# Kernel optimization log

Measured on AMD Instinct MI355X. Metric: run time of the kernel, lower is better.

Reference implementation:

```python
import jax, jax.numpy as jnp
from jax import lax
import numpy as np

B, L, D = 2, 2048, 768
DI, DS, DTR, K = 1536, 16, 48, 4  # d_inner, d_state, dt_rank, d_conv
EPS = 1e-5


def layernorm(x, g, b):
    mu = jnp.mean(x, axis=-1, keepdims=True)
    var = jnp.mean(jnp.square(x - mu), axis=-1, keepdims=True)
    return (x - mu) * lax.rsqrt(var + EPS) * g + b


def mamba(x, in_w, conv_w, conv_b, xproj_w, dt_w, dt_b, A_log, Dp, out_w):
    # x: [B, L, D]
    xz = x @ in_w.T                       # [B, L, 2*DI]
    xc, z = jnp.split(xz, 2, axis=-1)     # [B, L, DI] each
    # causal depthwise conv1d, kernel K, left pad K-1, truncate to L
    xp = jnp.pad(xc, ((0, 0), (K - 1, 0), (0, 0)))
    conv = conv_b + sum(xp[:, k:k + L, :] * conv_w[:, k] for k in range(K))
    xc = jax.nn.silu(conv)
    dbc = xc @ xproj_w.T                  # [B, L, DTR+2*DS]
    dt = dbc[..., :DTR]
    Bm = dbc[..., DTR:DTR + DS]           # [B, L, DS]
    Cm = dbc[..., DTR + DS:]              # [B, L, DS]
    dt = jax.nn.softplus(dt @ dt_w.T + dt_b)  # [B, L, DI]
    A = -jnp.exp(A_log)                   # [DI, DS]

    def step(h, inp):
        dt_t, B_t, C_t, x_t = inp         # [B,DI], [B,DS], [B,DS], [B,DI]
        dA = jnp.exp(dt_t[..., None] * A)               # [B, DI, DS]
        h = dA * h + (dt_t * x_t)[..., None] * B_t[:, None, :]
        y = jnp.einsum('bds,bs->bd', h, C_t)
        return h, y

    h0 = jnp.zeros((x.shape[0], DI, DS), x.dtype)
    _, ys = lax.scan(step, h0, (dt.transpose(1, 0, 2), Bm.transpose(1, 0, 2),
                                Cm.transpose(1, 0, 2), xc.transpose(1, 0, 2)))
    y = ys.transpose(1, 0, 2) + xc * Dp   # [B, L, DI]
    y = y * jax.nn.silu(z)
    return y @ out_w.T                    # [B, L, D]


def setup_inputs() -> dict:
    key = jax.random.key(0)
    ks = iter(jax.random.split(key, 40))
    r = lambda s, sc=0.02: jax.random.normal(next(ks), s, jnp.float32) * sc
    A0 = jnp.log(jnp.broadcast_to(jnp.arange(1, DS + 1, dtype=jnp.float32), (DI, DS)))
    def mamba_params(p):
        return {
            f'{p}_in_w': r((2 * DI, D)), f'{p}_conv_w': r((DI, K), 0.2),
            f'{p}_conv_b': jnp.zeros((DI,)), f'{p}_xproj_w': r((DTR + 2 * DS, DI)),
            f'{p}_dt_w': r((DI, DTR), 0.1), f'{p}_dt_b': jnp.zeros((DI,)),
            f'{p}_A_log': A0, f'{p}_D': jnp.ones((DI,)), f'{p}_out_w': r((D, DI)),
        }
    inp = {'x': jax.random.normal(next(ks), (B, L, D), jnp.float32),
           'norm_g': jnp.ones((D,)), 'norm_b': jnp.zeros((D,))}
    inp.update(mamba_params('f'))
    inp.update(mamba_params('b'))
    inp.update({'mix_w': r((D, 2 * D)), 'mix_b': jnp.zeros((D,)),
                'ffn_w1': r((4 * D, D)), 'ffn_b1': jnp.zeros((4 * D,)),
                'ffn_w2': r((D, 4 * D)), 'ffn_b2': jnp.zeros((D,)),
                'ffn_norm_g': jnp.ones((D,)), 'ffn_norm_b': jnp.zeros((D,))})
    return inp


def reference(x, norm_g, norm_b,
              f_in_w, f_conv_w, f_conv_b, f_xproj_w, f_dt_w, f_dt_b, f_A_log, f_D, f_out_w,
              b_in_w, b_conv_w, b_conv_b, b_xproj_w, b_dt_w, b_dt_b, b_A_log, b_D, b_out_w,
              mix_w, mix_b, ffn_w1, ffn_b1, ffn_w2, ffn_b2, ffn_norm_g, ffn_norm_b):
    residual = x
    xn = layernorm(x, norm_g, norm_b)
    xf = mamba(xn, f_in_w, f_conv_w, f_conv_b, f_xproj_w, f_dt_w, f_dt_b, f_A_log, f_D, f_out_w)
    xb = mamba(jnp.flip(xn, axis=1), b_in_w, b_conv_w, b_conv_b, b_xproj_w,
               b_dt_w, b_dt_b, b_A_log, b_D, b_out_w)
    xb = jnp.flip(xb, axis=1)
    xm = jnp.concatenate([xf, xb], axis=-1) @ mix_w.T + mix_b
    h = xm + residual
    hn = layernorm(h, ffn_norm_g, ffn_norm_b)
    ff = jax.nn.gelu(hn @ ffn_w1.T + ffn_b1) @ ffn_w2.T + ffn_b2  # dropout = eval identity
    return ff + h
```

## Files before the change

kernel.cpp:

```cpp
#include <hip/hip_runtime.h>
#include <hip/hip_bf16.h>
#include <math.h>

#define NB 2
#define LL 2048
#define DD 768
#define DI 1536
#define DS 16
#define MM (NB*LL)
#define TCH 64
#define NCH 32

typedef __hip_bfloat16 bf16;
typedef __attribute__((ext_vector_type(8))) __bf16 bf16x8;
typedef __attribute__((ext_vector_type(4))) float f32x4;

__device__ __forceinline__ float b2f(bf16 v){ return __bfloat162float(v); }
__device__ __forceinline__ bf16 f2b(float v){ return __float2bfloat16(v); }

__device__ __forceinline__ void un2(unsigned u, float& lo, float& hi){
  union {unsigned i; float f;} a, b;
  a.i = u << 16; b.i = u & 0xffff0000u;
  lo = a.f; hi = b.f;
}

__device__ __forceinline__ void async_cp16(const bf16* g, __bf16* l) {
  __builtin_amdgcn_global_load_lds((const __attribute__((address_space(1))) void*)g,
                                   (__attribute__((address_space(3))) void*)l, 16, 0, 0);
}

#define ACT_NONE 0
#define ACT_SOFTPLUS 1
#define ACT_GELU 2

__device__ __forceinline__ float apply_act(float v, int act) {
  if (act == ACT_SOFTPLUS) {
    v = (v > 15.f) ? v : log1pf(__expf(v));
  } else if (act == ACT_GELU) {
    float u = 0.7978845608028654f * (v + 0.044715f*v*v*v);
    v = 0.5f * v * (1.f + tanhf(u));
  }
  return v;
}

__global__ void gemm_kernel(const bf16* __restrict__ A, int lda,
                            const bf16* __restrict__ B, int ldb,
                            void* __restrict__ C, int ldc,
                            int N, int K,
                            const float* __restrict__ bias,
                            const float* __restrict__ addp, int ldadd,
                            int act, int f32out)
{
  __shared__ __bf16 As[128*64];
  __shared__ __bf16 Bs[128*64];
  const int tid  = threadIdx.x;
  const int lane = tid & 63, wave = tid >> 6;
  const int m0 = blockIdx.x * 128, n0 = blockIdx.y * 128;
  const int wm = wave & 1, wn = wave >> 1;

  const int srow = wave*32 + (lane >> 3);
  const int gsw  = (lane & 7) ^ ((lane >> 3) & 7);
  const int scol = gsw * 8;
  const bf16* Ag[4]; const bf16* Bg[4];
  __bf16 *AsW[4], *BsW[4];
  #pragma unroll
  for (int i = 0; i < 4; i++) {
    int ar = m0 + srow + i*8;
    Ag[i] = A + (size_t)ar * lda + scol;
    int br = n0 + srow + i*8; if (br > N-1) br = N-1;
    Bg[i] = B + (size_t)br * ldb + scol;
    AsW[i] = &As[(wave*32 + i*8)*64];
    BsW[i] = &Bs[(wave*32 + i*8)*64];
  }

  f32x4 acc[4][4] = {};
  const int arow = wm*64 + (lane & 15);
  const int brow = wn*64 + (lane & 15);
  const int rx = lane & 7;
  const int gq = lane >> 4;

  for (int kb = 0; kb < K; kb += 64) {
    __syncthreads();
    #pragma unroll
    for (int i = 0; i < 4; i++) {
      async_cp16(Ag[i] + kb, AsW[i]);
      async_cp16(Bg[i] + kb, BsW[i]);
    }
    __syncthreads();
    #pragma unroll
    for (int h = 0; h < 2; h++) {
      const int kk = ((h*4 + gq) ^ rx) * 8;
      bf16x8 af[4], bfr[4];
      #pragma unroll
      for (int i = 0; i < 4; i++) af[i]  = *(const bf16x8*)&As[(arow + i*16)*64 + kk];
      #pragma unroll
      for (int j = 0; j < 4; j++) bfr[j] = *(const bf16x8*)&Bs[(brow + j*16)*64 + kk];
      #pragma unroll
      for (int i = 0; i < 4; i++)
        #pragma unroll
        for (int j = 0; j < 4; j++)
          acc[i][j] = __builtin_amdgcn_mfma_f32_16x16x32_bf16(af[i], bfr[j], acc[i][j], 0, 0, 0);
    }
  }

  bf16*  Cb = (bf16*)C;
  float* Cf = (float*)C;
  #pragma unroll
  for (int i = 0; i < 4; i++) {
    int rbase = m0 + wm*64 + i*16 + (lane >> 4)*4;
    #pragma unroll
    for (int j = 0; j < 4; j++) {
      int col = n0 + wn*64 + j*16 + (lane & 15);
      if (col >= N) continue;
      float bv = bias ? bias[col] : 0.f;
      #pragma unroll
      for (int r = 0; r < 4; r++) {
        int row = rbase + r;
        float v = apply_act(acc[i][j][r] + bv, act);
        if (addp) v += addp[(size_t)row * ldadd + col];
        if (f32out) Cf[(size_t)row * ldc + col] = v;
        else        Cb[(size_t)row * ldc + col] = f2b(v);
      }
    }
  }
}

__global__ void gemm64_kernel(const bf16* __restrict__ A, int lda, size_t sA,
                              const bf16* __restrict__ B, int ldb, size_t sB,
                              void* __restrict__ C, int ldc, size_t sC,
                              int N, int K,
                              const float* __restrict__ bias0,
                              const float* __restrict__ bias1, int biasBase,
                              const float* __restrict__ addp, int ldadd,
                              int act, int f32out)
{
  __shared__ __bf16 As[64*64];
  __shared__ __bf16 Bs[64*64];
  const int tid  = threadIdx.x;
  const int lane = tid & 63, wave = tid >> 6;
  const int z = blockIdx.z;
  A += (size_t)z * sA;
  B += (size_t)z * sB;
  const float* bias = ((biasBase + z) ? bias1 : bias0);
  const int m0 = blockIdx.x * 64, n0 = blockIdx.y * 64;
  const int wm = wave & 1, wn = wave >> 1;

  const int srow = wave*16 + (lane >> 3);
  const int gsw  = (lane & 7) ^ ((lane >> 3) & 7);
  const int scol = gsw * 8;
  const bf16* Ag[2]; const bf16* Bg[2];
  __bf16 *AsW[2], *BsW[2];
  #pragma unroll
  for (int i = 0; i < 2; i++) {
    int ar = m0 + srow + i*8;
    Ag[i] = A + (size_t)ar * lda + scol;
    int br = n0 + srow + i*8; if (br > N-1) br = N-1;
    Bg[i] = B + (size_t)br * ldb + scol;
    AsW[i] = &As[(wave*16 + i*8)*64];
    BsW[i] = &Bs[(wave*16 + i*8)*64];
  }

  f32x4 acc[2][2] = {};
  const int arow = wm*32 + (lane & 15);
  const int brow = wn*32 + (lane & 15);
  const int rx = lane & 7;
  const int gq = lane >> 4;

  for (int kb = 0; kb < K; kb += 64) {
    __syncthreads();
    #pragma unroll
    for (int i = 0; i < 2; i++) {
      async_cp16(Ag[i] + kb, AsW[i]);
      async_cp16(Bg[i] + kb, BsW[i]);
    }
    __syncthreads();
    #pragma unroll
    for (int h = 0; h < 2; h++) {
      const int kk = ((h*4 + gq) ^ rx) * 8;
      bf16x8 af[2], bfr[2];
      #pragma unroll
      for (int i = 0; i < 2; i++) af[i]  = *(const bf16x8*)&As[(arow + i*16)*64 + kk];
      #pragma unroll
      for (int j = 0; j < 2; j++) bfr[j] = *(const bf16x8*)&Bs[(brow + j*16)*64 + kk];
      #pragma unroll
      for (int i = 0; i < 2; i++)
        #pragma unroll
        for (int j = 0; j < 2; j++)
          acc[i][j] = __builtin_amdgcn_mfma_f32_16x16x32_bf16(af[i], bfr[j], acc[i][j], 0, 0, 0);
    }
  }

  bf16*  Cb = (bf16*)C + z*sC;
  float* Cf = (float*)C + z*sC;
  #pragma unroll
  for (int i = 0; i < 2; i++) {
    int rbase = m0 + wm*32 + i*16 + (lane >> 4)*4;
    #pragma unroll
    for (int j = 0; j < 2; j++) {
      int col = n0 + wn*32 + j*16 + (lane & 15);
      if (col >= N) continue;
      float bv = bias ? bias[col] : 0.f;
      #pragma unroll
      for (int r = 0; r < 4; r++) {
        int row = rbase + r;
        float v = apply_act(acc[i][j][r] + bv, act);
        if (addp) v += addp[(size_t)row * ldadd + col];
        if (f32out) Cf[(size_t)row * ldc + col] = v;
        else        Cb[(size_t)row * ldc + col] = f2b(v);
      }
    }
  }
}

__global__ void ln_kernel(const float* __restrict__ x, const float* __restrict__ g,
                          const float* __restrict__ b, bf16* __restrict__ out)
{
  const int row = blockIdx.x;
  const int tid = threadIdx.x;
  const float* xr = x + (size_t)row * DD;
  float v[3], s = 0.f, s2 = 0.f;
  #pragma unroll
  for (int i = 0; i < 3; i++) {
    float f = xr[tid + i*256];
    v[i] = f; s += f; s2 += f*f;
  }
  #pragma unroll
  for (int o = 32; o > 0; o >>= 1) { s += __shfl_down(s, o, 64); s2 += __shfl_down(s2, o, 64); }
  __shared__ float ps[4], ps2[4];
  int wave = tid >> 6;
  if ((tid & 63) == 0) { ps[wave] = s; ps2[wave] = s2; }
  __syncthreads();
  s = ps[0]+ps[1]+ps[2]+ps[3]; s2 = ps2[0]+ps2[1]+ps2[2]+ps2[3];
  float mu = s * (1.f/DD);
  float var = s2 * (1.f/DD) - mu*mu;
  float rs = rsqrtf(var + 1e-5f);
  #pragma unroll
  for (int i = 0; i < 3; i++) {
    int c = tid + i*256;
    float o = (v[i] - mu) * rs * g[c] + b[c];
    out[(size_t)row * DD + c] = f2b(o);
  }
}

__global__ void conv_silu_kernel(const bf16* __restrict__ xz, int ldxz, int xzDirOff,
                                 const float* __restrict__ cw0, const float* __restrict__ cb0,
                                 const float* __restrict__ cw1, const float* __restrict__ cb1,
                                 bf16* __restrict__ xc, size_t sXc, int dirBase)
{
  int idx = blockIdx.x * 256 + threadIdx.x;
  int sIdx = (idx >= DI) ? 1 : 0;
  int d = idx - sIdx*DI;
  int dir = dirBase + sIdx;
  int row = blockIdx.y;
  int b = row >> 11, t = row & 2047;
  const float* cw = dir ? cw1 : cw0;
  const float* cb = dir ? cb1 : cb0;
  float acc = cb[d];
  float w0 = cw[d*4+0], w1 = cw[d*4+1], w2 = cw[d*4+2], w3 = cw[d*4+3];
  const bf16* base = xz + (size_t)(b*2048) * ldxz + sIdx*xzDirOff + d;
  if (dir == 0) {
    if (t >= 3) acc += b2f(base[(size_t)(t-3)*ldxz]) * w0;
    if (t >= 2) acc += b2f(base[(size_t)(t-2)*ldxz]) * w1;
    if (t >= 1) acc += b2f(base[(size_t)(t-1)*ldxz]) * w2;
    acc += b2f(base[(size_t)t*ldxz]) * w3;
  } else {
    if (t <= 2044) acc += b2f(base[(size_t)(t+3)*ldxz]) * w0;
    if (t <= 2045) acc += b2f(base[(size_t)(t+2)*ldxz]) * w1;
    if (t <= 2046) acc += b2f(base[(size_t)(t+1)*ldxz]) * w2;
    acc += b2f(base[(size_t)t*ldxz]) * w3;
  }
  float y = acc / (1.f + __expf(-acc));
  xc[sIdx*sXc + (size_t)row * DI + d] = f2b(y);
}

#define SZ_INW (2*DI*DD)
#define SZ_XP  (80*DI)
#define SZ_OUT (DD*DI)
#define SZ_DTW (DI*64)
#define SZ_AN  (DI*16)
#define SZ_MIX (2*DD*DD)
#define SZ_F1  (4*DD*DD)
__global__ void prep_all_kernel(const float* fi, const float* bi,
                                const float* fxp, const float* bxp,
                                const float* fo, const float* bo,
                                const float* fdt, const float* bdt,
                                const float* fa, const float* ba,
                                const float* mw, const float* f1, const float* f2,
                                bf16* w_in, bf16* w_xp2, bf16* w_out2, bf16* dtwp2,
                                float* An2, bf16* w_mix, bf16* w_f1, bf16* w_f2)
{
  int i = blockIdx.x * 256 + threadIdx.x;
  if (i < SZ_INW) { w_in[i] = f2b(fi[i]); return; }               i -= SZ_INW;
  if (i < SZ_INW) { w_in[SZ_INW + i] = f2b(bi[i]); return; }      i -= SZ_INW;
  if (i < SZ_XP)  { w_xp2[i] = f2b(fxp[i]); return; }             i -= SZ_XP;
  if (i < SZ_XP)  { w_xp2[SZ_XP + i] = f2b(bxp[i]); return; }     i -= SZ_XP;
  if (i < SZ_OUT) { w_out2[i] = f2b(fo[i]); return; }             i -= SZ_OUT;
  if (i < SZ_OUT) { w_out2[SZ_OUT + i] = f2b(bo[i]); return; }    i -= SZ_OUT;
  if (i < SZ_DTW) { int r=i>>6,c=i&63; dtwp2[i] = (c<48)?f2b(fdt[r*48+c]):f2b(0.f); return; } i -= SZ_DTW;
  if (i < SZ_DTW) { int r=i>>6,c=i&63; dtwp2[SZ_DTW+i] = (c<48)?f2b(bdt[r*48+c]):f2b(0.f); return; } i -= SZ_DTW;
  if (i < SZ_AN)  { int d=i>>4,s=i&15; An2[s*DI+d] = -__expf(fa[i]); return; } i -= SZ_AN;
  if (i < SZ_AN)  { int d=i>>4,s=i&15; An2[SZ_AN + s*DI+d] = -__expf(ba[i]); return; } i -= SZ_AN;
  if (i < SZ_MIX) { w_mix[i] = f2b(mw[i]); return; }              i -= SZ_MIX;
  if (i < SZ_F1)  { w_f1[i] = f2b(f1[i]); return; }               i -= SZ_F1;
  w_f2[i] = f2b(f2[i]);
}

__global__ void scan_partial(const bf16* __restrict__ dt, size_t sDt,
                             const bf16* __restrict__ xc, size_t sXc,
                             const bf16* __restrict__ dbc, size_t sDbc,
                             const float* __restrict__ An, size_t sAn,
                             float* __restrict__ Pp, float* __restrict__ Sp,
                             int dirBase)
{
  const int tid = threadIdx.x;
  const int sIdx = blockIdx.z >> 1, b = blockIdx.z & 1;
  const int dir = dirBase + sIdx;
  const int c = blockIdx.y;
  const int d = blockIdx.x * 256 + tid;
  dt  += sIdx*sDt; xc += sIdx*sXc; dbc += sIdx*sDbc;
  const int rowbase = b*2048 + c*TCH;
  __shared__ unsigned bcs[TCH*16];
  for (int i = tid; i < TCH*16; i += 256) {
    int r = i >> 4, dw = i & 15;
    bcs[i] = ((const unsigned*)(dbc + (size_t)(rowbase + r)*96 + 48))[dw];
  }
  __syncthreads();
  float A[16], P[16], g[16];
  #pragma unroll
  for (int s = 0; s < 16; s++) { A[s] = An[sIdx*sAn + s*DI + d]; P[s] = 1.f; g[s] = 0.f; }
  int ph0 = dir ? (TCH-1) : 0;
  float dtv = b2f(dt[(size_t)(rowbase+ph0)*DI + d]);
  float xv  = b2f(xc[(size_t)(rowbase+ph0)*DI + d]);
  for (int t = 0; t < TCH; t++) {
    const int ph = dir ? (TCH-1-t) : t;
    const int tn = (t+1 < TCH) ? t+1 : t;
    const int phn = dir ? (TCH-1-tn) : tn;
    float dtn = b2f(dt[(size_t)(rowbase+phn)*DI + d]);
    float xvn = b2f(xc[(size_t)(rowbase+phn)*DI + d]);
    unsigned ub[8];
    *(uint4*)&ub[0] = *(const uint4*)&bcs[ph*16];
    *(uint4*)&ub[4] = *(const uint4*)&bcs[ph*16 + 4];
    float Bv[16];
    #pragma unroll
    for (int k = 0; k < 8; k++) un2(ub[k], Bv[2*k], Bv[2*k+1]);
    float u = dtv * xv;
    #pragma unroll
    for (int s = 0; s < 16; s++) {
      float dA = __expf(dtv * A[s]);
      P[s] *= dA;
      g[s] = dA * g[s] + u * Bv[s];
    }
    dtv = dtn; xv = xvn;
  }
  size_t base = ((((size_t)sIdx*NB + b)*NCH + c)*DI + d) * 16;
  #pragma unroll
  for (int s = 0; s < 16; s++) { Pp[base+s] = P[s]; Sp[base+s] = g[s]; }
}

__global__ void scan_combine(const float* __restrict__ Pp, const float* __restrict__ Sp,
                             float* __restrict__ h0, int dirBase)
{
  const int j = blockIdx.x * 256 + threadIdx.x;
  const int b = blockIdx.y;
  const int sIdx = blockIdx.z;
  const int dir = dirBase + sIdx;
  float h = 0.f;
  for (int k = 0; k < NCH; k++) {
    int c = dir ? (NCH-1-k) : k;
    size_t idx = (((size_t)sIdx*NB + b)*NCH + c)*DI*16 + j;
    h0[idx] = h;
    h = Pp[idx]*h + Sp[idx];
  }
}

__global__ void scan_final(const bf16* __restrict__ dt, size_t sDt,
                           const bf16* __restrict__ xc, size_t sXc,
                           const bf16* __restrict__ dbc, size_t sDbc,
                           const bf16* __restrict__ xz, int ldxz, int xzDirOff,
                           const float* __restrict__ An, size_t sAn,
                           const float* __restrict__ Dp0, const float* __restrict__ Dp1,
                           const float* __restrict__ h0,
                           bf16* __restrict__ yout, size_t sY, int dirBase)
{
  const int tid = threadIdx.x;
  const int sIdx = blockIdx.z >> 1, b = blockIdx.z & 1;
  const int dir = dirBase + sIdx;
  const int c = blockIdx.y;
  const int d = blockIdx.x * 256 + tid;
  dt += sIdx*sDt; xc += sIdx*sXc; dbc += sIdx*sDbc; yout += sIdx*sY;
  const float* Dp = dir ? Dp1 : Dp0;
  const int rowbase = b*2048 + c*TCH;
  __shared__ unsigned bcs[TCH*16];
  for (int i = tid; i < TCH*16; i += 256) {
    int r = i >> 4, dw = i & 15;
    bcs[i] = ((const unsigned*)(dbc + (size_t)(rowbase + r)*96 + 48))[dw];
  }
  __syncthreads();
  float A[16], h[16];
  size_t hbase = ((((size_t)sIdx*NB + b)*NCH + c)*DI + d) * 16;
  #pragma unroll
  for (int s = 0; s < 16; s++) { A[s] = An[sIdx*sAn + s*DI + d]; h[s] = h0[hbase+s]; }
  const float Dd = Dp[d];
  const bf16* zp = xz + sIdx*xzDirOff + DI + d;
  int ph0 = dir ? (TCH-1) : 0;
  float dtv = b2f(dt[(size_t)(rowbase+ph0)*DI + d]);
  float xv  = b2f(xc[(size_t)(rowbase+ph0)*DI + d]);
  float zv  = b2f(zp[(size_t)(rowbase+ph0)*ldxz]);
  for (int t = 0; t < TCH; t++) {
    const int ph = dir ? (TCH-1-t) : t;
    const int row = rowbase + ph;
    const int tn = (t+1 < TCH) ? t+1 : t;
    const int phn = dir ? (TCH-1-tn) : tn;
    float dtn = b2f(dt[(size_t)(rowbase+phn)*DI + d]);
    float xvn = b2f(xc[(size_t)(rowbase+phn)*DI + d]);
    float zvn = b2f(zp[(size_t)(rowbase+phn)*ldxz]);
    unsigned ub[8], uc[8];
    *(uint4*)&ub[0] = *(const uint4*)&bcs[ph*16];
    *(uint4*)&ub[4] = *(const uint4*)&bcs[ph*16 + 4];
    *(uint4*)&uc[0] = *(const uint4*)&bcs[ph*16 + 8];
    *(uint4*)&uc[4] = *(const uint4*)&bcs[ph*16 + 12];
    float Bv[16], Cv[16];
    #pragma unroll
    for (int k = 0; k < 8; k++) { un2(ub[k], Bv[2*k], Bv[2*k+1]); un2(uc[k], Cv[2*k], Cv[2*k+1]); }
    float u = dtv * xv;
    float y = 0.f;
    #pragma unroll
    for (int s = 0; s < 16; s++) {
      float dA = __expf(dtv * A[s]);
      h[s] = dA * h[s] + u * Bv[s];
      y += h[s] * Cv[s];
    }
    float yg = (y + xv * Dd) * (zv / (1.f + __expf(-zv)));
    yout[(size_t)row*DI + d] = f2b(yg);
    dtv = dtn; xv = xvn; zv = zvn;
  }
}

extern "C" void kernel_launch(void* const* d_in, const int* in_sizes, int n_in,
                              void* d_out, int out_size, void* d_ws, size_t ws_size,
                              hipStream_t stream)
{
  const float* x      = (const float*)d_in[0];
  const float* norm_g = (const float*)d_in[1];
  const float* norm_b = (const float*)d_in[2];
  const float* fi  = (const float*)d_in[3];
  const float* fcw = (const float*)d_in[4];
  const float* fcb = (const float*)d_in[5];
  const float* fxp = (const float*)d_in[6];
  const float* fdt = (const float*)d_in[7];
  const float* fdb = (const float*)d_in[8];
  const float* fa  = (const float*)d_in[9];
  const float* fD  = (const float*)d_in[10];
  const float* fo  = (const float*)d_in[11];
  const float* bi  = (const float*)d_in[12];
  const float* bcw = (const float*)d_in[13];
  const float* bcb = (const float*)d_in[14];
  const float* bxp = (const float*)d_in[15];
  const float* bdt = (const float*)d_in[16];
  const float* bdb = (const float*)d_in[17];
  const float* ba  = (const float*)d_in[18];
  const float* bD  = (const float*)d_in[19];
  const float* bo  = (const float*)d_in[20];
  const float* mix_w  = (const float*)d_in[21];
  const float* mix_b  = (const float*)d_in[22];
  const float* ffn_w1 = (const float*)d_in[23];
  const float* ffn_b1 = (const float*)d_in[24];
  const float* ffn_w2 = (const float*)d_in[25];
  const float* ffn_b2 = (const float*)d_in[26];
  const float* ffn_ng = (const float*)d_in[27];
  const float* ffn_nb = (const float*)d_in[28];

  auto al = [](size_t x){ return (x + 255) & ~(size_t)255; };
  const size_t fixedB =
      al((size_t)2*SZ_AN*4) + al((size_t)2*SZ_DTW*2) + al((size_t)2*SZ_INW*2) +
      al((size_t)2*SZ_XP*2) + al((size_t)2*SZ_OUT*2) + al((size_t)SZ_MIX*2) +
      al((size_t)SZ_F1*2) + al((size_t)SZ_F1*2) + al((size_t)MM*DD*2) + al((size_t)MM*DI*2);
  const size_t concB = fixedB + al((size_t)MM*2*DI*2*2) + 2*al((size_t)2*MM*DI*2) +
      al((size_t)2*MM*96*2) + 3*al((size_t)2*NB*NCH*DI*16*4);
  const bool conc = (ws_size >= concB);

  size_t o = 0;
  char* wsb = (char*)d_ws;
  auto nxt = [&](size_t bytes) -> char* {
    char* p = wsb + o; o += (bytes + 255) & ~(size_t)255; return p;
  };
  float* An2   = (float*)nxt((size_t)2*SZ_AN*4);
  bf16*  dtwp2 = (bf16*) nxt((size_t)2*SZ_DTW*2);
  bf16*  w_in  = (bf16*) nxt((size_t)2*SZ_INW*2);
  bf16*  w_xp2 = (bf16*) nxt((size_t)2*SZ_XP*2);
  bf16*  w_out2= (bf16*) nxt((size_t)2*SZ_OUT*2);
  bf16*  w_mix = (bf16*) nxt((size_t)SZ_MIX*2);
  bf16*  w_f1  = (bf16*) nxt((size_t)SZ_F1*2);
  bf16*  w_f2  = (bf16*) nxt((size_t)SZ_F1*2);
  bf16*  xn    = (bf16*) nxt((size_t)MM*DD*2);
  bf16*  xfb   = (bf16*) nxt((size_t)MM*DI*2);

  bf16 *xz, *xc, *dtb, *dbc;  float *Pp, *Sp, *h0, *hbuf;
  int ldxz, xzDirOff;
  size_t sXc, sDbc, sDt;
  if (conc) {
    xz  = (bf16*) nxt((size_t)MM*2*DI*2*2);
    xc  = (bf16*) nxt((size_t)2*MM*DI*2);
    dtb = (bf16*) nxt((size_t)2*MM*DI*2);
    dbc = (bf16*) nxt((size_t)2*MM*96*2);
    Pp  = (float*)nxt((size_t)2*NB*NCH*DI*16*4);
    Sp  = (float*)nxt((size_t)2*NB*NCH*DI*16*4);
    h0  = (float*)nxt((size_t)2*NB*NCH*DI*16*4);
    hbuf = Pp;
    ldxz = 2*2*DI; xzDirOff = 2*DI;
    sXc = (size_t)MM*DI; sDbc = (size_t)MM*96; sDt = (size_t)MM*DI;
  } else {
    xz  = (bf16*) nxt((size_t)MM*2*DI*2);
    xc  = (bf16*) nxt((size_t)MM*DI*2);
    dtb = (bf16*) nxt((size_t)MM*DI*2);
    dbc = (bf16*) nxt((size_t)MM*96*2);
    Pp  = (float*)nxt((size_t)NB*NCH*DI*16*4);
    Sp  = (float*)nxt((size_t)NB*NCH*DI*16*4);
    h0  = (float*)nxt((size_t)NB*NCH*DI*16*4);
    hbuf = (float*)dtb;
    ldxz = 2*DI; xzDirOff = 0;
    sXc = 0; sDbc = 0; sDt = 0;
  }
  bf16* hn = xn;
  bf16* a1 = xz;

  const int prepN = 2*SZ_INW + 2*SZ_XP + 2*SZ_OUT + 2*SZ_DTW + 2*SZ_AN + SZ_MIX + 2*SZ_F1;
  prep_all_kernel<<<(prepN + 255)/256, 256, 0, stream>>>(
      fi, bi, fxp, bxp, fo, bo, fdt, bdt, fa, ba, mix_w, ffn_w1, ffn_w2,
      w_in, w_xp2, w_out2, dtwp2, An2, w_mix, w_f1, w_f2);

  ln_kernel<<<MM, 256, 0, stream>>>(x, norm_g, norm_b, xn);

  if (conc) {
    gemm_kernel<<<dim3(32, 48), 256, 0, stream>>>(xn, DD, w_in, DD, xz, ldxz,
                                                  2*2*DI, DD, nullptr, nullptr, 0,
                                                  ACT_NONE, 0);
    conv_silu_kernel<<<dim3(12, MM), 256, 0, stream>>>(xz, ldxz, xzDirOff,
                                                       fcw, fcb, bcw, bcb, xc, sXc, 0);
    gemm64_kernel<<<dim3(64, 2, 2), 256, 0, stream>>>(xc, DI, sXc, w_xp2, DI, (size_t)SZ_XP,
                                                      dbc, 96, sDbc, 80, DI,
                                                      nullptr, nullptr, 0, nullptr, 0, ACT_NONE, 0);
    gemm64_kernel<<<dim3(64, 24, 2), 256, 0, stream>>>(dbc, 96, sDbc, dtwp2, 64, (size_t)SZ_DTW,
                                                       dtb, DI, sDt, DI, 64,
                                                       fdb, bdb, 0, nullptr, 0, ACT_SOFTPLUS, 0);
    scan_partial<<<dim3(DI/256, NCH, 4), 256, 0, stream>>>(dtb, sDt, xc, sXc, dbc, sDbc,
                                                           An2, (size_t)SZ_AN, Pp, Sp, 0);
    scan_combine<<<dim3(DI*16/256, NB, 2), 256, 0, stream>>>(Pp, Sp, h0, 0);
    scan_final<<<dim3(DI/256, NCH, 4), 256, 0, stream>>>(dtb, sDt, xc, sXc, dbc, sDbc,
                                                         xz, ldxz, xzDirOff, An2, (size_t)SZ_AN,
                                                         fD, bD, h0, xc, sXc, 0);
    gemm64_kernel<<<dim3(64, 12, 2), 256, 0, stream>>>(xc, DI, sXc, w_out2, DI, (size_t)SZ_OUT,
                                                       xfb, 2*DD, (size_t)DD, DD, DI,
                                                       nullptr, nullptr, 0, nullptr, 0, ACT_NONE, 0);
  } else {
    for (int dir = 0; dir < 2; ++dir) {
      gemm_kernel<<<dim3(32, 24), 256, 0, stream>>>(xn, DD, w_in + (size_t)dir*SZ_INW, DD,
                                                    xz, ldxz, 2*DI, DD, nullptr, nullptr, 0,
                                                    ACT_NONE, 0);
      conv_silu_kernel<<<dim3(6, MM), 256, 0, stream>>>(xz, ldxz, 0,
                                                        fcw, fcb, bcw, bcb, xc, 0, dir);
      gemm64_kernel<<<dim3(64, 2, 1), 256, 0, stream>>>(xc, DI, 0, w_xp2 + (size_t)dir*SZ_XP, DI, 0,
                                                        dbc, 96, 0, 80, DI,
                                                        nullptr, nullptr, 0, nullptr, 0, ACT_NONE, 0);
      gemm64_kernel<<<dim3(64, 24, 1), 256, 0, stream>>>(dbc, 96, 0, dtwp2 + (size_t)dir*SZ_DTW, 64, 0,
                                                         dtb, DI, 0, DI, 64,
                                                         fdb, bdb, dir, nullptr, 0, ACT_SOFTPLUS, 0);
      scan_partial<<<dim3(DI/256, NCH, 2), 256, 0, stream>>>(dtb, 0, xc, 0, dbc, 0,
                                                             An2 + (size_t)dir*SZ_AN, 0, Pp, Sp, dir);
      scan_combine<<<dim3(DI*16/256, NB, 1), 256, 0, stream>>>(Pp, Sp, h0, dir);
      scan_final<<<dim3(DI/256, NCH, 2), 256, 0, stream>>>(dtb, 0, xc, 0, dbc, 0,
                                                           xz, ldxz, 0, An2 + (size_t)dir*SZ_AN, 0,
                                                           fD, bD, h0, xc, 0, dir);
      gemm64_kernel<<<dim3(64, 12, 1), 256, 0, stream>>>(xc, DI, 0, w_out2 + (size_t)dir*SZ_OUT, DI, 0,
                                                         (void*)((bf16*)xfb + dir*DD), 2*DD, 0, DD, DI,
                                                         nullptr, nullptr, 0, nullptr, 0, ACT_NONE, 0);
    }
  }

  gemm64_kernel<<<dim3(64, 12, 1), 256, 0, stream>>>(xfb, 2*DD, 0, w_mix, 2*DD, 0,
                                                     hbuf, DD, 0, DD, 2*DD,
                                                     mix_b, mix_b, 0, x, DD, ACT_NONE, 1);
  ln_kernel<<<MM, 256, 0, stream>>>(hbuf, ffn_ng, ffn_nb, hn);
  gemm_kernel<<<dim3(32, 24), 256, 0, stream>>>(hn, DD, w_f1, DD, a1, 4*DD,
                                                4*DD, DD, ffn_b1, nullptr, 0, ACT_GELU, 0);
  gemm64_kernel<<<dim3(64, 12, 1), 256, 0, stream>>>(a1, 4*DD, 0, w_f2, 4*DD, 0,
                                                     d_out, DD, 0, DD, 4*DD,
                                                     ffn_b2, ffn_b2, 0, hbuf, DD, ACT_NONE, 1);
}
```

Before: 617.9 us.

## Double-buffer shared-memory tiles in GEMM kernels to prefetch next K block

Both GEMM kernels now allocate two shared-memory stages for the A and B tiles. The first K block is loaded before the loop, and each iteration issues async copies of the next K block into the other stage before running MFMAs on the current one. One of the two barriers per iteration is removed, so global-to-LDS latency can overlap with compute. This doubles LDS use per block, which may lower occupancy, and correctness depends on the async copies having completed when the barrier passes.

```diff
diff --git a/kernel.cpp b/kernel.cpp
--- a/kernel.cpp
+++ b/kernel.cpp
@@ -51,8 +51,8 @@
                             const float* __restrict__ addp, int ldadd,
                             int act, int f32out)
 {
-  __shared__ __bf16 As[128*64];
-  __shared__ __bf16 Bs[128*64];
+  __shared__ __bf16 As[2*128*64];
+  __shared__ __bf16 Bs[2*128*64];
   const int tid  = threadIdx.x;
   const int lane = tid & 63, wave = tid >> 6;
   const int m0 = blockIdx.x * 128, n0 = blockIdx.y * 128;
@@ -62,15 +62,15 @@
   const int gsw  = (lane & 7) ^ ((lane >> 3) & 7);
   const int scol = gsw * 8;
   const bf16* Ag[4]; const bf16* Bg[4];
-  __bf16 *AsW[4], *BsW[4];
+  int aoff[4], boff[4];
   #pragma unroll
   for (int i = 0; i < 4; i++) {
     int ar = m0 + srow + i*8;
     Ag[i] = A + (size_t)ar * lda + scol;
     int br = n0 + srow + i*8; if (br > N-1) br = N-1;
     Bg[i] = B + (size_t)br * ldb + scol;
-    AsW[i] = &As[(wave*32 + i*8)*64];
-    BsW[i] = &Bs[(wave*32 + i*8)*64];
+    aoff[i] = (wave*32 + i*8)*64;
+    boff[i] = (wave*32 + i*8)*64;
   }
 
   f32x4 acc[4][4] = {};
@@ -79,28 +79,39 @@
   const int rx = lane & 7;
   const int gq = lane >> 4;
 
+  #pragma unroll
+  for (int i = 0; i < 4; i++) {
+    async_cp16(Ag[i], &As[aoff[i]]);
+    async_cp16(Bg[i], &Bs[boff[i]]);
+  }
+  int p = 0;
   for (int kb = 0; kb < K; kb += 64) {
     __syncthreads();
-    #pragma unroll
-    for (int i = 0; i < 4; i++) {
-      async_cp16(Ag[i] + kb, AsW[i]);
-      async_cp16(Bg[i] + kb, BsW[i]);
-    }
-    __syncthreads();
+    const int q = p ^ 1;
+    if (kb + 64 < K) {
+      const int qo = q * (128*64);
+      #pragma unroll
+      for (int i = 0; i < 4; i++) {
+        async_cp16(Ag[i] + kb + 64, &As[qo + aoff[i]]);
+        async_cp16(Bg[i] + kb + 64, &Bs[qo + boff[i]]);
+      }
+    }
+    const int po = p * (128*64);
     #pragma unroll
     for (int h = 0; h < 2; h++) {
       const int kk = ((h*4 + gq) ^ rx) * 8;
       bf16x8 af[4], bfr[4];
       #pragma unroll
-      for (int i = 0; i < 4; i++) af[i]  = *(const bf16x8*)&As[(arow + i*16)*64 + kk];
-      #pragma unroll
-      for (int j = 0; j < 4; j++) bfr[j] = *(const bf16x8*)&Bs[(brow + j*16)*64 + kk];
+      for (int i = 0; i < 4; i++) af[i]  = *(const bf16x8*)&As[po + (arow + i*16)*64 + kk];
+      #pragma unroll
+      for (int j = 0; j < 4; j++) bfr[j] = *(const bf16x8*)&Bs[po + (brow + j*16)*64 + kk];
       #pragma unroll
       for (int i = 0; i < 4; i++)
         #pragma unroll
         for (int j = 0; j < 4; j++)
           acc[i][j] = __builtin_amdgcn_mfma_f32_16x16x32_bf16(af[i], bfr[j], acc[i][j], 0, 0, 0);
     }
+    p = q;
   }
 
   bf16*  Cb = (bf16*)C;
@@ -134,8 +145,8 @@
                               const float* __restrict__ addp, int ldadd,
                               int act, int f32out)
 {
-  __shared__ __bf16 As[64*64];
-  __shared__ __bf16 Bs[64*64];
+  __shared__ __bf16 As[2*64*64];
+  __shared__ __bf16 Bs[2*64*64];
   const int tid  = threadIdx.x;
   const int lane = tid & 63, wave = tid >> 6;
   const int z = blockIdx.z;
@@ -149,15 +160,15 @@
   const int gsw  = (lane & 7) ^ ((lane >> 3) & 7);
   const int scol = gsw * 8;
   const bf16* Ag[2]; const bf16* Bg[2];
-  __bf16 *AsW[2], *BsW[2];
+  int aoff[2], boff[2];
   #pragma unroll
   for (int i = 0; i < 2; i++) {
     int ar = m0 + srow + i*8;
     Ag[i] = A + (size_t)ar * lda + scol;
     int br = n0 + srow + i*8; if (br > N-1) br = N-1;
     Bg[i] = B + (size_t)br * ldb + scol;
-    AsW[i] = &As[(wave*16 + i*8)*64];
-    BsW[i] = &Bs[(wave*16 + i*8)*64];
+    aoff[i] = (wave*16 + i*8)*64;
+    boff[i] = (wave*16 + i*8)*64;
   }
 
   f32x4 acc[2][2] = {};
@@ -166,28 +177,39 @@
   const int rx = lane & 7;
   const int gq = lane >> 4;
 
+  #pragma unroll
+  for (int i = 0; i < 2; i++) {
+    async_cp16(Ag[i], &As[aoff[i]]);
+    async_cp16(Bg[i], &Bs[boff[i]]);
+  }
+  int p = 0;
   for (int kb = 0; kb < K; kb += 64) {
     __syncthreads();
-    #pragma unroll
-    for (int i = 0; i < 2; i++) {
-      async_cp16(Ag[i] + kb, AsW[i]);
-      async_cp16(Bg[i] + kb, BsW[i]);
-    }
-    __syncthreads();
+    const int q = p ^ 1;
+    if (kb + 64 < K) {
+      const int qo = q * (64*64);
+      #pragma unroll
+      for (int i = 0; i < 2; i++) {
+        async_cp16(Ag[i] + kb + 64, &As[qo + aoff[i]]);
+        async_cp16(Bg[i] + kb + 64, &Bs[qo + boff[i]]);
+      }
+    }
+    const int po = p * (64*64);
     #pragma unroll
     for (int h = 0; h < 2; h++) {
       const int kk = ((h*4 + gq) ^ rx) * 8;
       bf16x8 af[2], bfr[2];
       #pragma unroll
-      for (int i = 0; i < 2; i++) af[i]  = *(const bf16x8*)&As[(arow + i*16)*64 + kk];
-      #pragma unroll
-      for (int j = 0; j < 2; j++) bfr[j] = *(const bf16x8*)&Bs[(brow + j*16)*64 + kk];
+      for (int i = 0; i < 2; i++) af[i]  = *(const bf16x8*)&As[po + (arow + i*16)*64 + kk];
+      #pragma unroll
+      for (int j = 0; j < 2; j++) bfr[j] = *(const bf16x8*)&Bs[po + (brow + j*16)*64 + kk];
       #pragma unroll
       for (int i = 0; i < 2; i++)
         #pragma unroll
         for (int j = 0; j < 2; j++)
           acc[i][j] = __builtin_amdgcn_mfma_f32_16x16x32_bf16(af[i], bfr[j], acc[i][j], 0, 0, 0);
     }
+    p = q;
   }
 
   bf16*  Cb = (bf16*)C + z*sC;
```

Measured after the change: 692.7 us. 1.12x slower.
